# Kernel tuning notes

Measured on AMD Instinct MI355X. Metric: run time of the kernel, lower is better.

Reference implementation:

```python
import jax, jax.numpy as jnp
import numpy as np

NUM_CLASSES = 2
THRESHOLD = 0.5
NEGPOS_RATIO = 3
VAR0, VAR1 = 0.1, 0.2  # self.variance = [0.1, 0.2]


def point_form(priors):
    # [cx,cy,w,h] -> [xmin,ymin,xmax,ymax]
    return jnp.concatenate([priors[:, :2] - priors[:, 2:] / 2,
                            priors[:, :2] + priors[:, 2:] / 2], axis=1)


def jaccard(a, b):
    # a: [O,4], b: [P,4] point-form -> IoU [O,P]
    tl = jnp.maximum(a[:, None, :2], b[None, :, :2])
    br = jnp.minimum(a[:, None, 2:], b[None, :, 2:])
    wh = jnp.clip(br - tl, 0.0)
    inter = wh[..., 0] * wh[..., 1]
    area_a = ((a[:, 2] - a[:, 0]) * (a[:, 3] - a[:, 1]))[:, None]
    area_b = ((b[:, 2] - b[:, 0]) * (b[:, 3] - b[:, 1]))[None, :]
    return inter / (area_a + area_b - inter)


def encode(matched, priors):
    # matched: [P,4] point-form GT, priors: [P,4] center-size
    g_cxcy = ((matched[:, :2] + matched[:, 2:]) / 2 - priors[:, :2]) / (VAR0 * priors[:, 2:])
    g_wh = jnp.log((matched[:, 2:] - matched[:, :2]) / priors[:, 2:]) / VAR1
    return jnp.concatenate([g_cxcy, g_wh], axis=1)


def match_one(truths, labels, priors):
    # truths: [O,4], labels: [O], priors: [P,4]
    O = truths.shape[0]
    overlaps = jaccard(truths, point_form(priors))          # [O,P]
    best_prior_idx = jnp.argmax(overlaps, axis=1)           # [O] best prior per GT
    best_truth_overlap = jnp.max(overlaps, axis=0)          # [P]
    best_truth_idx = jnp.argmax(overlaps, axis=0)           # [P]
    # ensure each GT keeps its best prior
    best_truth_overlap = best_truth_overlap.at[best_prior_idx].set(2.0)
    best_truth_idx = best_truth_idx.at[best_prior_idx].set(jnp.arange(O))
    matches = truths[best_truth_idx]                        # [P,4]
    conf = labels[best_truth_idx].astype(jnp.int32)         # head label == 1
    conf = jnp.where(best_truth_overlap < THRESHOLD, 0, conf)
    loc = encode(matches, priors)                           # [P,4]
    return loc, conf


def setup_inputs() -> dict:
    key = jax.random.key(0)
    k1, k2, k3, k4, k5, k6 = jax.random.split(key, 6)
    B, P, O = 32, 32768, 32
    loc_data = jax.random.normal(k1, (B, P, 3), jnp.float32) * 0.1
    conf_data = jax.random.normal(k2, (B, P, 2), jnp.float32)
    cxy = jax.random.uniform(k3, (P, 2), jnp.float32, 0.1, 0.9)
    wh = jax.random.uniform(k4, (P, 2), jnp.float32, 0.05, 0.2)
    priors = jnp.concatenate([cxy, wh], axis=1)
    xy1 = jax.random.uniform(k5, (B, O, 2), jnp.float32, 0.0, 0.7)
    twh = jax.random.uniform(k6, (B, O, 2), jnp.float32, 0.05, 0.25)
    targets = jnp.concatenate([xy1, xy1 + twh, jnp.ones((B, O, 1), jnp.float32)], axis=2)
    return {"loc_data": loc_data, "conf_data": conf_data, "priors": priors, "targets": targets}


def reference(loc_data, conf_data, priors, targets):
    B, P, _ = loc_data.shape
    # convert_coord: [cx, cy, gw] -> [cx, cy, gw, gw]
    quard = jnp.stack([loc_data[..., 0], loc_data[..., 1],
                       loc_data[..., 2], loc_data[..., 2]], axis=-1)  # [B,P,4]
    truths = targets[..., :4]
    labels = targets[..., 4]
    loc_t, conf_t = jax.vmap(lambda t, l: match_one(t, l, priors))(truths, labels)
    pos = conf_t > 0                                         # [B,P]
    # localization smooth-L1 over positives (sum reduction)
    d = quard - loc_t
    ad = jnp.abs(d)
    sl1 = jnp.where(ad < 1.0, 0.5 * d * d, ad - 0.5)
    loss_l = jnp.sum(sl1 * pos[..., None].astype(sl1.dtype))
    # per-prior CE for hard-negative mining
    lse = jax.nn.logsumexp(conf_data, axis=-1)               # [B,P]
    picked = jnp.take_along_axis(conf_data, conf_t[..., None], axis=-1)[..., 0]
    ce = lse - picked                                        # [B,P]
    ce_mine = jnp.where(pos, 0.0, ce)
    # double argsort -> rank of each prior by mining loss (descending)
    loss_idx = jnp.argsort(-ce_mine, axis=1)
    idx_rank = jnp.argsort(loss_idx, axis=1)
    num_pos = jnp.sum(pos.astype(jnp.int32), axis=1, keepdims=True)  # [B,1]
    num_neg = jnp.minimum(NEGPOS_RATIO * num_pos, P - 1)
    neg = idx_rank < num_neg
    sel = jnp.logical_or(pos, neg)
    loss_c = jnp.sum(jnp.where(sel, ce, 0.0))
    N = jnp.sum(num_pos).astype(loss_l.dtype)
    return loss_l / N, loss_c / N
```

## Files before the change

kernel.cpp:

```cpp
#include <hip/hip_runtime.h>
#include <math.h>

#define Bn 32
#define Pn 32768
#define On 32
#define TPB 256
#define PPT 4
#define BP  (TPB * PPT)
#define NCHUNK (Pn / BP)


__device__ __forceinline__ unsigned long long shfl_down_u64(unsigned long long v, int off) {
    unsigned lo = (unsigned)(v & 0xFFFFFFFFull);
    unsigned hi = (unsigned)(v >> 32);
    lo = __shfl_down(lo, off, 64);
    hi = __shfl_down(hi, off, 64);
    return ((unsigned long long)hi << 32) | lo;
}

__global__ __launch_bounds__(256, 4) void matchAB(const float* __restrict__ loc,
                                                  const float2* __restrict__ conf2,
                                                  const float4* __restrict__ priors,
                                                  const float* __restrict__ targets,
                                                  unsigned long long* __restrict__ bpm,
                                                  unsigned* __restrict__ cnt,
                                                  float* __restrict__ ce_mine,
                                                  int* __restrict__ num_pos,
                                                  float* __restrict__ loss_l_t,
                                                  float* __restrict__ ce_t,
                                                  int* __restrict__ np_tot) {
    int b = blockIdx.y;
    int base = blockIdx.x * BP;
    int tid = threadIdx.x;
    int lane = tid & 63, wv = tid >> 6;

    __shared__ float4 tb[On];
    __shared__ float  ta[On], lb[On];
    __shared__ int    forced[BP];
    __shared__ float  sred[12];

#pragma unroll
    for (int j = 0; j < PPT; j++) forced[tid + 256 * j] = -1;
    if (tid < On) {
        const float* t = targets + ((size_t)b * On + tid) * 5;
        float x1 = t[0], y1 = t[1], x2 = t[2], y2 = t[3];
        tb[tid] = make_float4(x1, y1, x2, y2);
        ta[tid] = (x2 - x1) * (y2 - y1);
        lb[tid] = t[4];
    }
    __syncthreads();

    {
        float bI[8], bU[8];
        int   bp[8];
#pragma unroll
        for (int t = 0; t < 8; t++) { bI[t] = 0.f; bU[t] = 1.f; bp[t] = base + lane; }

#pragma unroll
        for (int h = 0; h < 2; h++) {
            float ax1[8], ay1[8], ax2[8], ay2[8], aa[8];
#pragma unroll
            for (int i = 0; i < 8; i++) {
                float4 pr = priors[base + lane + 64 * (h * 8 + i)];
                ax1[i] = pr.x - pr.z * 0.5f; ay1[i] = pr.y - pr.w * 0.5f;
                ax2[i] = pr.x + pr.z * 0.5f; ay2[i] = pr.y + pr.w * 0.5f;
                aa[i]  = (ax2[i] - ax1[i]) * (ay2[i] - ay1[i]);
            }
#pragma unroll
            for (int t = 0; t < 8; t++) {
                int o = wv * 8 + t;
                float4 tt = tb[o];
                float  a  = ta[o];
#pragma unroll
                for (int i = 0; i < 8; i++) {
                    float ix1 = fmaxf(tt.x, ax1[i]), iy1 = fmaxf(tt.y, ay1[i]);
                    float ix2 = fminf(tt.z, ax2[i]), iy2 = fminf(tt.w, ay2[i]);
                    float iw = fmaxf(ix2 - ix1, 0.f), ih = fmaxf(iy2 - iy1, 0.f);
                    float I = iw * ih;
                    float U = a + aa[i] - I;
                    if (I * bU[t] > bI[t] * U) {
                        bI[t] = I; bU[t] = U; bp[t] = base + lane + 64 * (h * 8 + i);
                    }
                }
            }
        }

        unsigned long long key[8];
#pragma unroll
        for (int t = 0; t < 8; t++) {
            float iou = bI[t] / bU[t];
            key[t] = ((unsigned long long)__float_as_uint(iou) << 32)
                   | (unsigned)(Pn - 1 - bp[t]);
        }
#pragma unroll
        for (int off = 32; off > 0; off >>= 1) {
            unsigned long long other[8];
#pragma unroll
            for (int t = 0; t < 8; t++) other[t] = shfl_down_u64(key[t], off);
#pragma unroll
            for (int t = 0; t < 8; t++) if (other[t] > key[t]) key[t] = other[t];
        }
        if (lane == 0) {
#pragma unroll
            for (int t = 0; t < 8; t++)
                atomicMax(&bpm[b * On + wv * 8 + t], key[t]);
        }
    }

    float2 cc[PPT];
#pragma unroll
    for (int j = 0; j < PPT; j++) cc[j] = conf2[(size_t)b * Pn + base + tid + 256 * j];

    __syncthreads();

    if (tid == 0) {
        atomicAdd(&cnt[b], 1u);
        while (atomicAdd(&cnt[b], 0u) < (unsigned)NCHUNK) {
            __builtin_amdgcn_s_sleep(16);
        }
    }
    __syncthreads();

    int sp = -1;
    if (tid < On)
        sp = Pn - 1 - (int)(atomicMax(&bpm[b * On + tid], 0ull) & 0xFFFFFFFFull);
    if (tid < On && sp >= base && sp < base + BP)
        atomicMax(&forced[sp - base], tid);
    __syncthreads();

    float px1[PPT], py1[PPT], px2[PPT], py2[PPT], ab[PPT], pcx[PPT], pcy[PPT], pw[PPT], ph[PPT];
#pragma unroll
    for (int j = 0; j < PPT; j++) {
        float4 pr = priors[base + tid + 256 * j];
        pcx[j] = pr.x; pcy[j] = pr.y; pw[j] = pr.z; ph[j] = pr.w;
        px1[j] = pr.x - pr.z * 0.5f; py1[j] = pr.y - pr.w * 0.5f;
        px2[j] = pr.x + pr.z * 0.5f; py2[j] = pr.y + pr.w * 0.5f;
        ab[j]  = (px2[j] - px1[j]) * (py2[j] - py1[j]);
    }

    float bIc[PPT][2], bUc[PPT][2];
    int   bxc[PPT][2];
#pragma unroll
    for (int j = 0; j < PPT; j++)
#pragma unroll
        for (int h = 0; h < 2; h++) { bIc[j][h] = 0.f; bUc[j][h] = 1.f; bxc[j][h] = h * 16; }

#pragma unroll 2
    for (int o16 = 0; o16 < 16; o16++) {
#pragma unroll
        for (int h = 0; h < 2; h++) {
            int o = h * 16 + o16;
            float4 tt = tb[o];
            float  a  = ta[o];
#pragma unroll
            for (int j = 0; j < PPT; j++) {
                float ix1 = fmaxf(tt.x, px1[j]), iy1 = fmaxf(tt.y, py1[j]);
                float ix2 = fminf(tt.z, px2[j]), iy2 = fminf(tt.w, py2[j]);
                float iw = fmaxf(ix2 - ix1, 0.f), ih = fmaxf(iy2 - iy1, 0.f);
                float I = iw * ih;
                float U = a + ab[j] - I;
                if (I * bUc[j][h] > bIc[j][h] * U) { bIc[j][h] = I; bUc[j][h] = U; bxc[j][h] = o; }
            }
        }
    }
    float bI[PPT], bU[PPT];
    int   bx[PPT];
#pragma unroll
    for (int j = 0; j < PPT; j++) {
        bI[j] = bIc[j][0]; bU[j] = bUc[j][0]; bx[j] = bxc[j][0];
        if (bIc[j][1] * bU[j] > bI[j] * bUc[j][1]) { bI[j] = bIc[j][1]; bU[j] = bUc[j][1]; bx[j] = bxc[j][1]; }
    }

    float ll_s = 0.f, pce_s = 0.f, cnt_s = 0.f;
#pragma unroll
    for (int j = 0; j < PPT; j++) {
        int p = base + tid + 256 * j;
        int fo = forced[tid + 256 * j];
        int bidx = (fo >= 0) ? fo : bx[j];
        int cf;
        if (fo >= 0)                      cf = (int)lb[bidx];
        else if (bI[j] >= 0.5f * bU[j])   cf = (int)lb[bidx];
        else                              cf = 0;
        bool pos = cf > 0;

        if (pos) {
            float4 tt = tb[bidx];
            float g0 = ((tt.x + tt.z) * 0.5f - pcx[j]) / (0.1f * pw[j]);
            float g1 = ((tt.y + tt.w) * 0.5f - pcy[j]) / (0.1f * ph[j]);
            float g2 = __logf((tt.z - tt.x) / pw[j]) * 5.0f;
            float g3 = __logf((tt.w - tt.y) / ph[j]) * 5.0f;
            const float* lp = loc + ((size_t)b * Pn + p) * 3;
            float q0 = lp[0], q1 = lp[1], q2 = lp[2];
            float dd[4] = { q0 - g0, q1 - g1, q2 - g2, q2 - g3 };
#pragma unroll
            for (int i = 0; i < 4; i++) {
                float ad = fabsf(dd[i]);
                ll_s += (ad < 1.f) ? 0.5f * dd[i] * dd[i] : (ad - 0.5f);
            }
            cnt_s += 1.f;
        }

        float m = fmaxf(cc[j].x, cc[j].y);
        float lse = m + __logf(__expf(cc[j].x - m) + __expf(cc[j].y - m));
        float ce = lse - (cf ? cc[j].y : cc[j].x);
        if (pos) { pce_s += ce; ce = 0.f; }
        ce_mine[(size_t)b * Pn + p] = fmaxf(ce, 0.f);
    }

#pragma unroll
    for (int off = 32; off > 0; off >>= 1) {
        ll_s  += __shfl_down(ll_s,  off, 64);
        pce_s += __shfl_down(pce_s, off, 64);
        cnt_s += __shfl_down(cnt_s, off, 64);
    }
    if (lane == 0) { sred[wv * 3] = ll_s; sred[wv * 3 + 1] = pce_s; sred[wv * 3 + 2] = cnt_s; }
    __syncthreads();
    if (tid == 0) {
        float llr = 0, pcer = 0, cntr = 0;
        for (int w = 0; w < 4; w++) { llr += sred[w*3]; pcer += sred[w*3+1]; cntr += sred[w*3+2]; }
        if (llr != 0.f)  atomicAdd(loss_l_t, llr);
        if (pcer != 0.f) atomicAdd(ce_t, pcer);
        int c = (int)cntr;
        if (c) { atomicAdd(&num_pos[b], c); atomicAdd(np_tot, c); }
    }
}

__global__ __launch_bounds__(1024) void topk(const float* __restrict__ ce_mine,
                                             const int* __restrict__ num_pos,
                                             float* __restrict__ ce_t,
                                             const float* __restrict__ loss_l_t,
                                             const int* __restrict__ np_tot,
                                             unsigned* __restrict__ tick,
                                             float* __restrict__ out) {
    int b = blockIdx.x, tid = threadIdx.x;
    const float4* v4 = (const float4*)(ce_mine + (size_t)b * Pn);
    float4 r[8];
#pragma unroll
    for (int i = 0; i < 8; i++) r[i] = v4[i * 1024 + tid];

    int k = 3 * num_pos[b];
    if (k > Pn - 1) k = Pn - 1;

    __shared__ int hist[8192];
    __shared__ unsigned s_lo;
    __shared__ int s_ab;
    __shared__ float ssum[16];
    __shared__ int   scnt[16];

    int lane = tid & 63, wv = tid >> 6;

    if (k > 0) {
        unsigned LO = 0u;
        int AB = 0;

        const int SH[3] = {22, 11, 0};
        const int NB[3] = {512, 2048, 2048};

#pragma unroll
        for (int rd = 0; rd < 3; rd++) {
            int shift = SH[rd], nb = NB[rd];
#pragma unroll
            for (int i = 0; i < 8; i++) hist[tid + 1024 * i] = 0;
            __syncthreads();
            int* myh = hist + ((wv >> 2) << 11);
#pragma unroll
            for (int i = 0; i < 8; i++) {
                float4 rv = r[i];
                float vals[4] = {rv.x, rv.y, rv.z, rv.w};
#pragma unroll
                for (int q = 0; q < 4; q++) {
                    unsigned u = __float_as_uint(vals[q]);
                    unsigned bin = (u - LO) >> shift;
                    if (bin < (unsigned)nb) atomicAdd(&myh[bin], 1);
                }
            }
            __syncthreads();
            if (wv == 0) {
                int bpl = nb >> 6;
                int bb = lane * bpl;
                int lsum = 0;
                for (int q = 0; q < bpl; q++) {
                    int bin = bb + q;
                    lsum += hist[bin] + hist[2048 + bin] + hist[4096 + bin] + hist[6144 + bin];
                }
                int suf = lsum;
#pragma unroll
                for (int off = 1; off < 64; off <<= 1) {
                    int o = __shfl(suf, (lane + off) & 63, 64);
                    suf += ((lane + off) < 64) ? o : 0;
                }
                int kk = k - AB;
                if (suf >= kk && (suf - lsum) < kk) {
                    int acc = suf - lsum;
                    for (int q = bpl - 1; q >= 0; q--) {
                        int bin = bb + q;
                        int hc = hist[bin] + hist[2048 + bin] + hist[4096 + bin] + hist[6144 + bin];
                        acc += hc;
                        if (acc >= kk) {
                            s_lo = LO + ((unsigned)bin << shift);
                            s_ab = AB + (acc - hc);
                            break;
                        }
                    }
                }
            }
            __syncthreads();
            LO = s_lo; AB = s_ab;
        }
        float tau = __uint_as_float(LO);
        float s = 0.f; int c = 0;
#pragma unroll
        for (int i = 0; i < 8; i++) {
            if (r[i].x > tau) { s += r[i].x; c++; }
            if (r[i].y > tau) { s += r[i].y; c++; }
            if (r[i].z > tau) { s += r[i].z; c++; }
            if (r[i].w > tau) { s += r[i].w; c++; }
        }
#pragma unroll
        for (int off = 32; off > 0; off >>= 1) {
            s += __shfl_down(s, off, 64);
            c += __shfl_down(c, off, 64);
        }
        if (lane == 0) { ssum[wv] = s; scnt[wv] = c; }
        __syncthreads();
        if (tid == 0) {
            float st = 0.f; int ct = 0;
            for (int w = 0; w < 16; w++) { st += ssum[w]; ct += scnt[w]; }
            atomicAdd(ce_t, st + (float)(k - ct) * tau);
        }
    }

    if (tid == 0) {
        __threadfence();
        unsigned done = atomicAdd(tick, 1u);
        if (done == (unsigned)(Bn - 1)) {
            float N  = (float)atomicAdd((int*)np_tot, 0);
            float ll = atomicAdd((float*)loss_l_t, 0.f);
            float ce = atomicAdd(ce_t, 0.f);
            out[0] = ll / N;
            out[1] = ce / N;
        }
    }
}

extern "C" void kernel_launch(void* const* d_in, const int* in_sizes, int n_in,
                              void* d_out, int out_size, void* d_ws, size_t ws_size,
                              hipStream_t stream) {
    const float* loc     = (const float*)d_in[0];
    const float* conf    = (const float*)d_in[1];
    const float* priors  = (const float*)d_in[2];
    const float* targets = (const float*)d_in[3];
    float* out = (float*)d_out;

    char* ws = (char*)d_ws;
    unsigned long long* bpm = (unsigned long long*)ws;
    int*   num_pos  = (int*)(ws + 8192);
    float* loss_l_t = (float*)(ws + 8320);
    float* ce_t     = (float*)(ws + 8324);
    int*   np_tot   = (int*)(ws + 8328);
    unsigned* tick  = (unsigned*)(ws + 8332);
    unsigned* cnt   = (unsigned*)(ws + 8336);
    float* ce_mine  = (float*)(ws + 16384);

    hipMemsetAsync(ws, 0, 16384, stream);

    hipLaunchKernelGGL(matchAB, dim3(NCHUNK, Bn), dim3(256), 0, stream,
                       loc, (const float2*)conf, (const float4*)priors, targets,
                       bpm, cnt, ce_mine, num_pos, loss_l_t, ce_t, np_tot);
    hipLaunchKernelGGL(topk, dim3(Bn), dim3(1024), 0, stream,
                       ce_mine, num_pos, ce_t, loss_l_t, np_tot, tick, out);
}
```

Measured before the change: 187.8 us.

## Replace inter-block spin barrier with split passes and forced-match delta correction

Removes the global spin-wait barrier in the match kernel that made every chunk wait until all chunks had published their best-prior atomics. The grid now has a z dimension: z=0 blocks compute the per-GT best prior, and z=1 blocks compute the per-prior match without forced overrides. The topk kernel then applies the forced matches as a delta correction to loss_l, ce, num_pos and ce_mine before selection. This exposes more parallelism and avoids spinning, but it adds a small serial fixup in topk and relies on the delta logic correctly handling duplicate forced priors.

```diff
diff --git a/kernel.cpp b/kernel.cpp
--- a/kernel.cpp
+++ b/kernel.cpp
@@ -18,17 +18,16 @@
     return ((unsigned long long)hi << 32) | lo;
 }
 
-__global__ __launch_bounds__(256, 4) void matchAB(const float* __restrict__ loc,
-                                                  const float2* __restrict__ conf2,
-                                                  const float4* __restrict__ priors,
-                                                  const float* __restrict__ targets,
-                                                  unsigned long long* __restrict__ bpm,
-                                                  unsigned* __restrict__ cnt,
-                                                  float* __restrict__ ce_mine,
-                                                  int* __restrict__ num_pos,
-                                                  float* __restrict__ loss_l_t,
-                                                  float* __restrict__ ce_t,
-                                                  int* __restrict__ np_tot) {
+__global__ __launch_bounds__(256) void match(const float* __restrict__ loc,
+                                             const float2* __restrict__ conf2,
+                                             const float4* __restrict__ priors,
+                                             const float* __restrict__ targets,
+                                             unsigned long long* __restrict__ bpm,
+                                             float* __restrict__ ce_mine,
+                                             int* __restrict__ num_pos,
+                                             float* __restrict__ loss_l_t,
+                                             float* __restrict__ ce_t,
+                                             int* __restrict__ np_tot) {
     int b = blockIdx.y;
     int base = blockIdx.x * BP;
     int tid = threadIdx.x;
@@ -36,11 +35,8 @@
 
     __shared__ float4 tb[On];
     __shared__ float  ta[On], lb[On];
-    __shared__ int    forced[BP];
     __shared__ float  sred[12];
 
-#pragma unroll
-    for (int j = 0; j < PPT; j++) forced[tid + 256 * j] = -1;
     if (tid < On) {
         const float* t = targets + ((size_t)b * On + tid) * 5;
         float x1 = t[0], y1 = t[1], x2 = t[2], y2 = t[3];
@@ -50,7 +46,7 @@
     }
     __syncthreads();
 
-    {
+    if (blockIdx.z == 0) {
         float bI[8], bU[8];
         int   bp[8];
 #pragma unroll
@@ -84,7 +80,6 @@
                 }
             }
         }
-
         unsigned long long key[8];
 #pragma unroll
         for (int t = 0; t < 8; t++) {
@@ -105,28 +100,12 @@
             for (int t = 0; t < 8; t++)
                 atomicMax(&bpm[b * On + wv * 8 + t], key[t]);
         }
+        return;
     }
 
     float2 cc[PPT];
 #pragma unroll
     for (int j = 0; j < PPT; j++) cc[j] = conf2[(size_t)b * Pn + base + tid + 256 * j];
-
-    __syncthreads();
-
-    if (tid == 0) {
-        atomicAdd(&cnt[b], 1u);
-        while (atomicAdd(&cnt[b], 0u) < (unsigned)NCHUNK) {
-            __builtin_amdgcn_s_sleep(16);
-        }
-    }
-    __syncthreads();
-
-    int sp = -1;
-    if (tid < On)
-        sp = Pn - 1 - (int)(atomicMax(&bpm[b * On + tid], 0ull) & 0xFFFFFFFFull);
-    if (tid < On && sp >= base && sp < base + BP)
-        atomicMax(&forced[sp - base], tid);
-    __syncthreads();
 
     float px1[PPT], py1[PPT], px2[PPT], py2[PPT], ab[PPT], pcx[PPT], pcy[PPT], pw[PPT], ph[PPT];
 #pragma unroll
@@ -175,12 +154,8 @@
 #pragma unroll
     for (int j = 0; j < PPT; j++) {
         int p = base + tid + 256 * j;
-        int fo = forced[tid + 256 * j];
-        int bidx = (fo >= 0) ? fo : bx[j];
-        int cf;
-        if (fo >= 0)                      cf = (int)lb[bidx];
-        else if (bI[j] >= 0.5f * bU[j])   cf = (int)lb[bidx];
-        else                              cf = 0;
+        int bidx = bx[j];
+        int cf = (bI[j] >= 0.5f * bU[j]) ? (int)lb[bidx] : 0;
         bool pos = cf > 0;
 
         if (pos) {
@@ -225,29 +200,126 @@
     }
 }
 
-__global__ __launch_bounds__(1024) void topk(const float* __restrict__ ce_mine,
-                                             const int* __restrict__ num_pos,
+__global__ __launch_bounds__(1024) void topk(const float* __restrict__ loc,
+                                             const float2* __restrict__ conf2,
+                                             const float4* __restrict__ priors,
+                                             const float* __restrict__ targets,
+                                             const unsigned long long* __restrict__ bpm,
+                                             float* __restrict__ ce_mine,
+                                             int* __restrict__ num_pos,
                                              float* __restrict__ ce_t,
-                                             const float* __restrict__ loss_l_t,
-                                             const int* __restrict__ np_tot,
+                                             float* __restrict__ loss_l_t,
+                                             int* __restrict__ np_tot,
                                              unsigned* __restrict__ tick,
                                              float* __restrict__ out) {
     int b = blockIdx.x, tid = threadIdx.x;
-    const float4* v4 = (const float4*)(ce_mine + (size_t)b * Pn);
-    float4 r[8];
-#pragma unroll
-    for (int i = 0; i < 8; i++) r[i] = v4[i * 1024 + tid];
-
-    int k = 3 * num_pos[b];
-    if (k > Pn - 1) k = Pn - 1;
+    int lane = tid & 63, wv = tid >> 6;
 
     __shared__ int hist[8192];
+    __shared__ float4 ftb[On];
+    __shared__ float  fta[On], flb[On];
+    __shared__ int    fpr[On];
+    __shared__ int    s_k;
     __shared__ unsigned s_lo;
     __shared__ int s_ab;
     __shared__ float ssum[16];
     __shared__ int   scnt[16];
 
-    int lane = tid & 63, wv = tid >> 6;
+    if (tid < On) {
+        const float* t = targets + ((size_t)b * On + tid) * 5;
+        float x1 = t[0], y1 = t[1], x2 = t[2], y2 = t[3];
+        ftb[tid] = make_float4(x1, y1, x2, y2);
+        fta[tid] = (x2 - x1) * (y2 - y1);
+        flb[tid] = t[4];
+        fpr[tid] = Pn - 1 - (int)(bpm[b * On + tid] & 0xFFFFFFFFull);
+    }
+    __syncthreads();
+    if (tid < On) {
+        int pt = fpr[tid];
+        bool winner = true;
+        for (int t2 = tid + 1; t2 < On; t2++) if (fpr[t2] == pt) winner = false;
+        if (winner) {
+            float4 pr = priors[pt];
+            float pcx = pr.x, pcy = pr.y, pw = pr.z, ph = pr.w;
+            float px1 = pr.x - pr.z * 0.5f, py1 = pr.y - pr.w * 0.5f;
+            float px2 = pr.x + pr.z * 0.5f, py2 = pr.y + pr.w * 0.5f;
+            float ab  = (px2 - px1) * (py2 - py1);
+            float bIc[2] = {0.f, 0.f}, bUc[2] = {1.f, 1.f};
+            int   bxc[2] = {0, 16};
+            for (int o16 = 0; o16 < 16; o16++) {
+                for (int h = 0; h < 2; h++) {
+                    int o = h * 16 + o16;
+                    float4 tt = ftb[o];
+                    float  a  = fta[o];
+                    float ix1 = fmaxf(tt.x, px1), iy1 = fmaxf(tt.y, py1);
+                    float ix2 = fminf(tt.z, px2), iy2 = fminf(tt.w, py2);
+                    float iw = fmaxf(ix2 - ix1, 0.f), ih = fmaxf(iy2 - iy1, 0.f);
+                    float I = iw * ih;
+                    float U = a + ab - I;
+                    if (I * bUc[h] > bIc[h] * U) { bIc[h] = I; bUc[h] = U; bxc[h] = o; }
+                }
+            }
+            float bI = bIc[0], bU = bUc[0]; int bx = bxc[0];
+            if (bIc[1] * bU > bI * bUc[1]) { bI = bIc[1]; bU = bUc[1]; bx = bxc[1]; }
+
+            int  cf_old  = (bI >= 0.5f * bU) ? (int)flb[bx] : 0;
+            bool pos_old = cf_old > 0;
+            int  cf_new  = (int)flb[tid];
+            bool pos_new = cf_new > 0;
+
+            float2 cc = conf2[(size_t)b * Pn + pt];
+            float m = fmaxf(cc.x, cc.y);
+            float lse = m + __logf(__expf(cc.x - m) + __expf(cc.y - m));
+            float ce_old = lse - (cf_old ? cc.y : cc.x);
+            float ce_new = lse - (cf_new ? cc.y : cc.x);
+
+            const float* lp = loc + ((size_t)b * Pn + pt) * 3;
+            float q0 = lp[0], q1 = lp[1], q2 = lp[2];
+            float ll_old = 0.f, ll_new = 0.f;
+            if (pos_old) {
+                float4 tt = ftb[bx];
+                float g0 = ((tt.x + tt.z) * 0.5f - pcx) / (0.1f * pw);
+                float g1 = ((tt.y + tt.w) * 0.5f - pcy) / (0.1f * ph);
+                float g2 = __logf((tt.z - tt.x) / pw) * 5.0f;
+                float g3 = __logf((tt.w - tt.y) / ph) * 5.0f;
+                float dd[4] = { q0 - g0, q1 - g1, q2 - g2, q2 - g3 };
+                for (int i = 0; i < 4; i++) {
+                    float ad = fabsf(dd[i]);
+                    ll_old += (ad < 1.f) ? 0.5f * dd[i] * dd[i] : (ad - 0.5f);
+                }
+            }
+            if (pos_new) {
+                float4 tt = ftb[tid];
+                float g0 = ((tt.x + tt.z) * 0.5f - pcx) / (0.1f * pw);
+                float g1 = ((tt.y + tt.w) * 0.5f - pcy) / (0.1f * ph);
+                float g2 = __logf((tt.z - tt.x) / pw) * 5.0f;
+                float g3 = __logf((tt.w - tt.y) / ph) * 5.0f;
+                float dd[4] = { q0 - g0, q1 - g1, q2 - g2, q2 - g3 };
+                for (int i = 0; i < 4; i++) {
+                    float ad = fabsf(dd[i]);
+                    ll_new += (ad < 1.f) ? 0.5f * dd[i] * dd[i] : (ad - 0.5f);
+                }
+            }
+            float dll = ll_new - ll_old;
+            float dce = (pos_new ? ce_new : 0.f) - (pos_old ? ce_old : 0.f);
+            int   dnp = (pos_new ? 1 : 0) - (pos_old ? 1 : 0);
+            if (dll != 0.f) atomicAdd(loss_l_t, dll);
+            if (dce != 0.f) atomicAdd(ce_t, dce);
+            if (dnp) { atomicAdd(&num_pos[b], dnp); atomicAdd(np_tot, dnp); }
+            float cm_new = pos_new ? 0.f : fmaxf(ce_new, 0.f);
+            ce_mine[(size_t)b * Pn + pt] = cm_new;
+        }
+    }
+    if (tid == 0) s_k = atomicAdd(&num_pos[b], 0);
+    __syncthreads();
+
+    const float4* v4 = (const float4*)(ce_mine + (size_t)b * Pn);
+    float4 r[8];
+#pragma unroll
+    for (int i = 0; i < 8; i++) r[i] = v4[i * 1024 + tid];
+
+    int k = 3 * s_k;
+    if (k > Pn - 1) k = Pn - 1;
 
     if (k > 0) {
         unsigned LO = 0u;
@@ -334,8 +406,8 @@
         __threadfence();
         unsigned done = atomicAdd(tick, 1u);
         if (done == (unsigned)(Bn - 1)) {
-            float N  = (float)atomicAdd((int*)np_tot, 0);
-            float ll = atomicAdd((float*)loss_l_t, 0.f);
+            float N  = (float)atomicAdd(np_tot, 0);
+            float ll = atomicAdd(loss_l_t, 0.f);
             float ce = atomicAdd(ce_t, 0.f);
             out[0] = ll / N;
             out[1] = ce / N;
@@ -359,14 +431,14 @@
     float* ce_t     = (float*)(ws + 8324);
     int*   np_tot   = (int*)(ws + 8328);
     unsigned* tick  = (unsigned*)(ws + 8332);
-    unsigned* cnt   = (unsigned*)(ws + 8336);
     float* ce_mine  = (float*)(ws + 16384);
 
     hipMemsetAsync(ws, 0, 16384, stream);
 
-    hipLaunchKernelGGL(matchAB, dim3(NCHUNK, Bn), dim3(256), 0, stream,
+    hipLaunchKernelGGL(match, dim3(NCHUNK, Bn, 2), dim3(256), 0, stream,
                        loc, (const float2*)conf, (const float4*)priors, targets,
-                       bpm, cnt, ce_mine, num_pos, loss_l_t, ce_t, np_tot);
+                       bpm, ce_mine, num_pos, loss_l_t, ce_t, np_tot);
     hipLaunchKernelGGL(topk, dim3(Bn), dim3(1024), 0, stream,
+                       loc, (const float2*)conf, (const float4*)priors, targets, bpm,
                        ce_mine, num_pos, ce_t, loss_l_t, np_tot, tick, out);
 }
```

After: 158.6 us. 15.5% less time.
